# Optimization experiments

Hardware: AMD Instinct MI355X
Metric: run time of the kernel (lower is better)

## Reference

```python
import jax, jax.numpy as jnp
import numpy as np

HID = 512
NB = 20
N = 65536
EPS = 1e-5


def layer_norm(x, g, b):
    m = jnp.mean(x, axis=-1, keepdims=True)
    v = jnp.mean(jnp.square(x - m), axis=-1, keepdims=True)
    return (x - m) * jax.lax.rsqrt(v + EPS) * g + b


def setup_inputs() -> dict:
    key = jax.random.key(0)
    ks = jax.random.split(key, 8)
    s = 0.02
    return {
        "x": jax.random.normal(ks[0], (N, 2), dtype=jnp.float32),
        "in_w": jax.random.normal(ks[1], (2, HID), dtype=jnp.float32) * s,
        "in_b": jnp.zeros((HID,), jnp.float32),
        "ln1_g": jnp.ones((NB, HID), jnp.float32),
        "ln1_b": jnp.zeros((NB, HID), jnp.float32),
        "fc1_w": jax.random.normal(ks[2], (NB, HID, HID), dtype=jnp.float32) * s,
        "fc1_b": jnp.zeros((NB, HID), jnp.float32),
        "ln2_g": jnp.ones((NB, HID), jnp.float32),
        "ln2_b": jnp.zeros((NB, HID), jnp.float32),
        "fc2_w": jax.random.normal(ks[3], (NB, HID, HID), dtype=jnp.float32) * s,
        "fc2_b": jnp.zeros((NB, HID), jnp.float32),
        "out_ln_g": jnp.ones((HID,), jnp.float32),
        "out_ln_b": jnp.zeros((HID,), jnp.float32),
        "out_w": jax.random.normal(ks[4], (HID, 1), dtype=jnp.float32) * s,
        "out_b": jnp.zeros((1,), jnp.float32),
    }


def reference(x, in_w, in_b, ln1_g, ln1_b, fc1_w, fc1_b, ln2_g, ln2_b,
              fc2_w, fc2_b, out_ln_g, out_ln_b, out_w, out_b):
    # in_proj + SiLU: [N,2] @ [2,HID]
    h = jax.nn.silu(x @ in_w + in_b)

    def block(h, p):
        g1, b1, w1, c1, g2, b2, w2, c2 = p
        t = jax.nn.silu(layer_norm(h, g1, b1) @ w1 + c1)
        t = layer_norm(t, g2, b2) @ w2 + c2
        return h + t, None

    h, _ = jax.lax.scan(block, h, (ln1_g, ln1_b, fc1_w, fc1_b,
                                   ln2_g, ln2_b, fc2_w, fc2_b))
    h = jax.nn.silu(layer_norm(h, out_ln_g, out_ln_b))
    return h @ out_w + out_b  # [N, 1]
```

## Files before the change

### kernel.cpp

```cpp
#include <hip/hip_runtime.h>
#include <hip/hip_bf16.h>


typedef float  fvec4 __attribute__((ext_vector_type(4)));
typedef __bf16 bvec8 __attribute__((ext_vector_type(8)));

#define HN_STRIDE 520
#define WCHUNK    16384
#define SMEM_BYTES (64*HN_STRIDE*2 + 64*8)
#define WPK_USHORTS ((size_t)20*2*16*WCHUNK)

__device__ __forceinline__ unsigned int f2bf(float v) {
    unsigned int u = __float_as_uint(v);
    return (u + 0x7fffu + ((u >> 16) & 1u)) >> 16;
}
__device__ __forceinline__ unsigned int pkbf(float a, float b) {
    __hip_bfloat162 t = __float22bfloat162_rn(make_float2(a, b));
    unsigned int r;
    __builtin_memcpy(&r, &t, 4);
    return r;
}
__device__ __forceinline__ float silu_f(float v) {
    return v * (1.0f / (1.0f + __expf(-v)));
}

__global__ __launch_bounds__(256) void pack_weights(
        const float* __restrict__ w1, const float* __restrict__ w2,
        const float* __restrict__ g1, const float* __restrict__ g2,
        unsigned short* __restrict__ pk) {
    int tid = blockIdx.x * 256 + threadIdx.x;
    int l  = tid & 63;
    int f  = tid >> 6;
    int t  = f & 1;
    int kc = (f >> 1) & 15;
    int w  = (f >> 5) & 15;
    int g  = (f >> 9) & 1;
    int b  = f >> 10;
    const float* src = g ? w2 : w1;
    const float* gs  = (g ? g2 : g1) + b * 512;
    int k0 = kc * 32 + (l >> 4) * 8;
    int n  = w * 32 + (l & 15) * 2 + t;
    const float* s = src + ((size_t)b * 512 + k0) * 512 + n;
    unsigned int r[4];
#pragma unroll
    for (int j = 0; j < 4; ++j) {
        float ga = gs[k0 + 2 * j];
        float gb = gs[k0 + 2 * j + 1];
        unsigned int lo = f2bf(ga * s[(size_t)(2*j) * 512]);
        unsigned int hi = f2bf(gb * s[(size_t)(2*j + 1) * 512]);
        r[j] = lo | (hi << 16);
    }
    *(uint4*)(pk + (size_t)tid * 8) = make_uint4(r[0], r[1], r[2], r[3]);
}

__global__ __launch_bounds__(512) void make_uv(
        const float* __restrict__ w1, const float* __restrict__ w2,
        const float* __restrict__ g1, const float* __restrict__ bl1,
        const float* __restrict__ cb1,
        const float* __restrict__ g2, const float* __restrict__ bl2,
        const float* __restrict__ cb2,
        float* __restrict__ uv) {
    int b = blockIdx.x >> 1, slot = blockIdx.x & 1, n = threadIdx.x;
    const float* W  = (slot ? w2 : w1) + (size_t)b * 512 * 512;
    const float* g  = (slot ? g2 : g1) + b * 512;
    const float* bl = (slot ? bl2 : bl1) + b * 512;
    const float* cb = (slot ? cb2 : cb1) + b * 512;
    float u = 0.f, v = 0.f;
    for (int j = 0; j < 512; ++j) {
        float wv = W[(size_t)j * 512 + n];
        u = fmaf(g[j], wv, u);
        v = fmaf(bl[j], wv, v);
    }
    uv[((b * 2 + slot) * 2 + 0) * 512 + n] = u;
    uv[((b * 2 + slot) * 2 + 1) * 512 + n] = v + cb[n];
}

__device__ __forceinline__ void acc_u32(unsigned int u, float& s, float& ss) {
    float lo = __uint_as_float(u << 16);
    float hi = __uint_as_float(u & 0xFFFF0000u);
    s += lo + hi;
    ss = __builtin_fmaf(lo, lo, ss);
    ss = __builtin_fmaf(hi, hi, ss);
}

__device__ __forceinline__ void gemm_red(
        fvec4 acc[4][2], const unsigned short* hn,
        const unsigned short* __restrict__ wp, uint4 pre0, uint4 pre1,
        float2* mv, int l, int c, int q, int tid) {
    const uint4* wp4 = (const uint4*)wp;
    const int r = tid >> 4, j = tid & 15;
    float s = 0.f, ss = 0.f;
#pragma unroll
    for (int kc = 0; kc < 16; ++kc) {
        bvec8 a[4], b0, b1;
#pragma unroll
        for (int rb = 0; rb < 4; ++rb)
            a[rb] = *(const bvec8*)(hn + (rb * 16 + c) * HN_STRIDE + kc * 32 + q * 8);
        if (kc == 0) {
            __builtin_memcpy(&b0, &pre0, 16);
            __builtin_memcpy(&b1, &pre1, 16);
        } else {
            uint4 r0 = wp4[(kc * 2 + 0) * 64 + l];
            uint4 r1 = wp4[(kc * 2 + 1) * 64 + l];
            __builtin_memcpy(&b0, &r0, 16);
            __builtin_memcpy(&b1, &r1, 16);
        }
        if (kc >= 4 && kc < 8) {
            uint4 pv = *(const uint4*)(hn + r * HN_STRIDE + (j + 16 * (kc - 4)) * 8);
            acc_u32(pv.x, s, ss); acc_u32(pv.y, s, ss);
            acc_u32(pv.z, s, ss); acc_u32(pv.w, s, ss);
        }
#pragma unroll
        for (int rb = 0; rb < 4; ++rb) {
            acc[rb][0] = __builtin_amdgcn_mfma_f32_16x16x32_bf16(a[rb], b0, acc[rb][0], 0, 0, 0);
            acc[rb][1] = __builtin_amdgcn_mfma_f32_16x16x32_bf16(a[rb], b1, acc[rb][1], 0, 0, 0);
        }
    }
    s += __shfl_xor(s, 1); ss += __shfl_xor(ss, 1);
    s += __shfl_xor(s, 2); ss += __shfl_xor(ss, 2);
    s += __shfl_xor(s, 4); ss += __shfl_xor(ss, 4);
    s += __shfl_xor(s, 8); ss += __shfl_xor(ss, 8);
    if (j == 0) {
        float mean = s * (1.f / 512.f);
        float var  = ss * (1.f / 512.f) - mean * mean;
        mv[r] = make_float2(mean, rsqrtf(var + 1e-5f));
    }
}

__device__ __forceinline__ void reduce_mv_hn(const unsigned short* hn,
                                             float2* mv, int tid) {
    int r = tid >> 4, j = tid & 15;
    float s = 0.f, ss = 0.f;
#pragma unroll
    for (int u = 0; u < 4; ++u) {
        uint4 pv = *(const uint4*)(hn + r * HN_STRIDE + (j + 16 * u) * 8);
        acc_u32(pv.x, s, ss); acc_u32(pv.y, s, ss);
        acc_u32(pv.z, s, ss); acc_u32(pv.w, s, ss);
    }
    s += __shfl_xor(s, 1); ss += __shfl_xor(ss, 1);
    s += __shfl_xor(s, 2); ss += __shfl_xor(ss, 2);
    s += __shfl_xor(s, 4); ss += __shfl_xor(ss, 4);
    s += __shfl_xor(s, 8); ss += __shfl_xor(ss, 8);
    if (j == 0) {
        float mean = s * (1.f / 512.f);
        float var  = ss * (1.f / 512.f) - mean * mean;
        mv[r] = make_float2(mean, rsqrtf(var + 1e-5f));
    }
}

__global__ __launch_bounds__(1024, 4) void mlp_fused(
        const float* __restrict__ x,
        const float* __restrict__ in_w,  const float* __restrict__ in_b,
        const float* __restrict__ out_ln_g, const float* __restrict__ out_ln_b,
        const float* __restrict__ out_w, const float* __restrict__ out_b,
        const unsigned short* __restrict__ wpk,
        const float* __restrict__ uv,
        float* __restrict__ out) {
    extern __shared__ char smem[];
    unsigned short* hn = (unsigned short*)smem;
    float* hnf = (float*)smem;
    float2* mv = (float2*)(smem + 64 * HN_STRIDE * 2);

    const int tid = threadIdx.x;
    const int w = tid >> 6;
    const int l = tid & 63, c = l & 15, q = l >> 4;
    const int colbase = w * 32 + c * 2;
    const int row0 = blockIdx.x * 64;

    float h[4][4][2];

    {
        float2 iw0 = *(const float2*)(in_w + colbase);
        float2 iw1 = *(const float2*)(in_w + 512 + colbase);
        float2 ib  = *(const float2*)(in_b + colbase);
#pragma unroll
        for (int rb = 0; rb < 4; ++rb)
#pragma unroll
            for (int i = 0; i < 4; ++i) {
                int row = rb * 16 + q * 4 + i;
                float2 xv = *(const float2*)(x + (size_t)(row0 + row) * 2);
                h[rb][i][0] = silu_f(xv.x * iw0.x + xv.y * iw1.x + ib.x);
                h[rb][i][1] = silu_f(xv.x * iw0.y + xv.y * iw1.y + ib.y);
            }
    }

    for (int b = 0; b < 20; ++b) {
        const unsigned short* wp1 = wpk + ((size_t)(b * 2 + 0) * 16 + w) * WCHUNK;
        const unsigned short* wp2 = wpk + ((size_t)(b * 2 + 1) * 16 + w) * WCHUNK;
        float2 u1  = *(const float2*)(uv + ((b * 2 + 0) * 2 + 0) * 512 + colbase);
        float2 vc1 = *(const float2*)(uv + ((b * 2 + 0) * 2 + 1) * 512 + colbase);
        float2 u2  = *(const float2*)(uv + ((b * 2 + 1) * 2 + 0) * 512 + colbase);
        float2 vc2 = *(const float2*)(uv + ((b * 2 + 1) * 2 + 1) * 512 + colbase);

        uint4 pre0 = ((const uint4*)wp1)[l];
        uint4 pre1 = ((const uint4*)wp1)[64 + l];
#pragma unroll
        for (int rb = 0; rb < 4; ++rb)
#pragma unroll
            for (int i = 0; i < 4; ++i) {
                int row = rb * 16 + q * 4 + i;
                *(unsigned int*)(hn + row * HN_STRIDE + colbase) =
                    pkbf(h[rb][i][0], h[rb][i][1]);
            }
        __syncthreads();

        fvec4 acc[4][2];
#pragma unroll
        for (int rb = 0; rb < 4; ++rb)
#pragma unroll
            for (int t = 0; t < 2; ++t) acc[rb][t] = (fvec4){0.f, 0.f, 0.f, 0.f};
        gemm_red(acc, hn, wp1, pre0, pre1, mv, l, c, q, tid);
        __syncthreads();

        pre0 = ((const uint4*)wp2)[l];
        pre1 = ((const uint4*)wp2)[64 + l];
#pragma unroll
        for (int rb = 0; rb < 4; ++rb)
#pragma unroll
            for (int i = 0; i < 4; ++i) {
                int row = rb * 16 + q * 4 + i;
                float2 m = mv[row];
                float minv = -m.x * m.y;
                float t0 = silu_f(__builtin_fmaf(acc[rb][0][i], m.y,
                                  __builtin_fmaf(minv, u1.x, vc1.x)));
                float t1 = silu_f(__builtin_fmaf(acc[rb][1][i], m.y,
                                  __builtin_fmaf(minv, u1.y, vc1.y)));
                *(unsigned int*)(hn + row * HN_STRIDE + colbase) = pkbf(t0, t1);
            }
        __syncthreads();

#pragma unroll
        for (int rb = 0; rb < 4; ++rb)
#pragma unroll
            for (int t = 0; t < 2; ++t) acc[rb][t] = (fvec4){0.f, 0.f, 0.f, 0.f};
        gemm_red(acc, hn, wp2, pre0, pre1, mv, l, c, q, tid);
        __syncthreads();

#pragma unroll
        for (int rb = 0; rb < 4; ++rb)
#pragma unroll
            for (int i = 0; i < 4; ++i) {
                int row = rb * 16 + q * 4 + i;
                float2 m = mv[row];
                float minv = -m.x * m.y;
                h[rb][i][0] = __builtin_fmaf(acc[rb][0][i], m.y,
                    h[rb][i][0] + __builtin_fmaf(minv, u2.x, vc2.x));
                h[rb][i][1] = __builtin_fmaf(acc[rb][1][i], m.y,
                    h[rb][i][1] + __builtin_fmaf(minv, u2.y, vc2.y));
            }
    }

#pragma unroll
    for (int rb = 0; rb < 4; ++rb)
#pragma unroll
        for (int i = 0; i < 4; ++i) {
            int row = rb * 16 + q * 4 + i;
            *(unsigned int*)(hn + row * HN_STRIDE + colbase) =
                pkbf(h[rb][i][0], h[rb][i][1]);
        }
    __syncthreads();
    reduce_mv_hn(hn, mv, tid);
    __syncthreads();
    {
        float2 og = *(const float2*)(out_ln_g + colbase);
        float2 ob = *(const float2*)(out_ln_b + colbase);
        float2 ow = *(const float2*)(out_w + colbase);
        const int pcol = w * 16 + c;
#pragma unroll
    for (int rb = 0; rb < 4; ++rb)
#pragma unroll
            for (int i = 0; i < 4; ++i) {
                int row = rb * 16 + q * 4 + i;
                float2 m = mv[row];
                float v0 = (h[rb][i][0] - m.x) * m.y * og.x + ob.x;
                float v1 = (h[rb][i][1] - m.x) * m.y * og.y + ob.y;
                hnf[pcol * 65 + row] = silu_f(v0) * ow.x + silu_f(v1) * ow.y;
            }
    }
    __syncthreads();
    {
        int r = tid >> 4, j = tid & 15;
        float s = 0.f;
#pragma unroll
        for (int u = 0; u < 16; ++u)
            s += hnf[(j + 16 * u) * 65 + r];
        s += __shfl_xor(s, 1);
        s += __shfl_xor(s, 2);
        s += __shfl_xor(s, 4);
        s += __shfl_xor(s, 8);
        if (j == 0) out[row0 + r] = s + out_b[0];
    }
}

extern "C" void kernel_launch(void* const* d_in, const int* in_sizes, int n_in,
                              void* d_out, int out_size, void* d_ws, size_t ws_size,
                              hipStream_t stream) {
    const float* x        = (const float*)d_in[0];
    const float* in_w     = (const float*)d_in[1];
    const float* in_b     = (const float*)d_in[2];
    const float* ln1_g    = (const float*)d_in[3];
    const float* ln1_b    = (const float*)d_in[4];
    const float* fc1_w    = (const float*)d_in[5];
    const float* fc1_b    = (const float*)d_in[6];
    const float* ln2_g    = (const float*)d_in[7];
    const float* ln2_b    = (const float*)d_in[8];
    const float* fc2_w    = (const float*)d_in[9];
    const float* fc2_b    = (const float*)d_in[10];
    const float* out_ln_g = (const float*)d_in[11];
    const float* out_ln_b = (const float*)d_in[12];
    const float* out_w    = (const float*)d_in[13];
    const float* out_b    = (const float*)d_in[14];
    float* out = (float*)d_out;
    unsigned short* wpk = (unsigned short*)d_ws;
    float* uv = (float*)((char*)d_ws + WPK_USHORTS * 2);

    (void)hipFuncSetAttribute((const void*)mlp_fused,
                              hipFuncAttributeMaxDynamicSharedMemorySize, SMEM_BYTES);

    pack_weights<<<5120, 256, 0, stream>>>(fc1_w, fc2_w, ln1_g, ln2_g, wpk);
    make_uv<<<40, 512, 0, stream>>>(fc1_w, fc2_w, ln1_g, ln1_b, fc1_b,
                                    ln2_g, ln2_b, fc2_b, uv);
    mlp_fused<<<1024, 1024, SMEM_BYTES, stream>>>(
        x, in_w, in_b, out_ln_g, out_ln_b, out_w, out_b, wpk, uv, out);
}
```

Before: 1.776 ms.

## Compute LayerNorm partial sums at emit time and prefetch next block weights

Each thread now computes partial sum and sum-of-squares for its two output values when writing activations, reduces them over 4 lanes with shuffles, and stores them to a new shared-memory plane. The GEMM and final reduction then read 64 partials per row instead of re-reading and unpacking the whole bf16 row. Statistics now come from fp32 values rather than bf16-rounded ones. The first weight chunk of the next block is also prefetched before the residual update. This trades extra shuffles and shared-memory footprint (which may affect occupancy) for fewer LDS reads and less ALU work in the GEMM loop.

Measured after the change: 2.754 ms. 55.0% more time.

```diff
diff --git a/kernel.cpp b/kernel.cpp
--- a/kernel.cpp
+++ b/kernel.cpp
@@ -6,8 +6,9 @@
 typedef __bf16 bvec8 __attribute__((ext_vector_type(8)));
 
 #define HN_STRIDE 520
+#define PL_STRIDE 66
 #define WCHUNK    16384
-#define SMEM_BYTES (64*HN_STRIDE*2 + 64*8)
+#define SMEM_BYTES (64*HN_STRIDE*2 + 64*PL_STRIDE*8 + 64*8)
 #define WPK_USHORTS ((size_t)20*2*16*WCHUNK)
 
 __device__ __forceinline__ unsigned int f2bf(float v) {
@@ -75,18 +76,10 @@
     uv[((b * 2 + slot) * 2 + 1) * 512 + n] = v + cb[n];
 }
 
-__device__ __forceinline__ void acc_u32(unsigned int u, float& s, float& ss) {
-    float lo = __uint_as_float(u << 16);
-    float hi = __uint_as_float(u & 0xFFFF0000u);
-    s += lo + hi;
-    ss = __builtin_fmaf(lo, lo, ss);
-    ss = __builtin_fmaf(hi, hi, ss);
-}
-
 __device__ __forceinline__ void gemm_red(
         fvec4 acc[4][2], const unsigned short* hn,
         const unsigned short* __restrict__ wp, uint4 pre0, uint4 pre1,
-        float2* mv, int l, int c, int q, int tid) {
+        const float2* plane2, float2* mv, int l, int c, int q, int tid) {
     const uint4* wp4 = (const uint4*)wp;
     const int r = tid >> 4, j = tid & 15;
     float s = 0.f, ss = 0.f;
@@ -105,10 +98,15 @@
             __builtin_memcpy(&b0, &r0, 16);
             __builtin_memcpy(&b1, &r1, 16);
         }
-        if (kc >= 4 && kc < 8) {
-            uint4 pv = *(const uint4*)(hn + r * HN_STRIDE + (j + 16 * (kc - 4)) * 8);
-            acc_u32(pv.x, s, ss); acc_u32(pv.y, s, ss);
-            acc_u32(pv.z, s, ss); acc_u32(pv.w, s, ss);
+        if (kc == 4) {
+            float2 p0 = plane2[r * PL_STRIDE + j * 4 + 0];
+            float2 p1 = plane2[r * PL_STRIDE + j * 4 + 1];
+            s += p0.x + p1.x; ss += p0.y + p1.y;
+        }
+        if (kc == 5) {
+            float2 p0 = plane2[r * PL_STRIDE + j * 4 + 2];
+            float2 p1 = plane2[r * PL_STRIDE + j * 4 + 3];
+            s += p0.x + p1.x; ss += p0.y + p1.y;
         }
 #pragma unroll
         for (int rb = 0; rb < 4; ++rb) {
@@ -127,15 +125,14 @@
     }
 }
 
-__device__ __forceinline__ void reduce_mv_hn(const unsigned short* hn,
-                                             float2* mv, int tid) {
+__device__ __forceinline__ void reduce_mv_plane(const float2* plane2,
+                                                float2* mv, int tid) {
     int r = tid >> 4, j = tid & 15;
     float s = 0.f, ss = 0.f;
 #pragma unroll
-    for (int u = 0; u < 4; ++u) {
-        uint4 pv = *(const uint4*)(hn + r * HN_STRIDE + (j + 16 * u) * 8);
-        acc_u32(pv.x, s, ss); acc_u32(pv.y, s, ss);
-        acc_u32(pv.z, s, ss); acc_u32(pv.w, s, ss);
+    for (int k = 0; k < 4; ++k) {
+        float2 p = plane2[r * PL_STRIDE + j * 4 + k];
+        s += p.x; ss += p.y;
     }
     s += __shfl_xor(s, 1); ss += __shfl_xor(ss, 1);
     s += __shfl_xor(s, 2); ss += __shfl_xor(ss, 2);
@@ -159,15 +156,27 @@
     extern __shared__ char smem[];
     unsigned short* hn = (unsigned short*)smem;
     float* hnf = (float*)smem;
-    float2* mv = (float2*)(smem + 64 * HN_STRIDE * 2);
+    float2* plane2 = (float2*)(smem + 64 * HN_STRIDE * 2);
+    float2* mv = (float2*)(smem + 64 * HN_STRIDE * 2 + 64 * PL_STRIDE * 8);
 
     const int tid = threadIdx.x;
     const int w = tid >> 6;
     const int l = tid & 63, c = l & 15, q = l >> 4;
     const int colbase = w * 32 + c * 2;
     const int row0 = blockIdx.x * 64;
+    const int grp = w * 4 + (c >> 2);
+    const bool gw = (c & 3) == 0;
 
     float h[4][4][2];
+
+    auto emit = [&](int row, float v0, float v1) {
+        *(unsigned int*)(hn + row * HN_STRIDE + colbase) = pkbf(v0, v1);
+        float s  = v0 + v1;
+        float ss = __builtin_fmaf(v0, v0, v1 * v1);
+        s += __shfl_xor(s, 1); ss += __shfl_xor(ss, 1);
+        s += __shfl_xor(s, 2); ss += __shfl_xor(ss, 2);
+        if (gw) plane2[row * PL_STRIDE + grp] = make_float2(s, ss);
+    };
 
     {
         float2 iw0 = *(const float2*)(in_w + colbase);
@@ -181,27 +190,22 @@
                 float2 xv = *(const float2*)(x + (size_t)(row0 + row) * 2);
                 h[rb][i][0] = silu_f(xv.x * iw0.x + xv.y * iw1.x + ib.x);
                 h[rb][i][1] = silu_f(xv.x * iw0.y + xv.y * iw1.y + ib.y);
+                emit(row, h[rb][i][0], h[rb][i][1]);
             }
     }
+    uint4 pre0 = ((const uint4*)(wpk + ((size_t)0 * 16 + w) * WCHUNK))[l];
+    uint4 pre1 = ((const uint4*)(wpk + ((size_t)0 * 16 + w) * WCHUNK))[64 + l];
 
     for (int b = 0; b < 20; ++b) {
         const unsigned short* wp1 = wpk + ((size_t)(b * 2 + 0) * 16 + w) * WCHUNK;
         const unsigned short* wp2 = wpk + ((size_t)(b * 2 + 1) * 16 + w) * WCHUNK;
+        int bn = (b < 19) ? (b + 1) * 2 : 38;
+        const unsigned short* wpn = wpk + ((size_t)bn * 16 + w) * WCHUNK;
         float2 u1  = *(const float2*)(uv + ((b * 2 + 0) * 2 + 0) * 512 + colbase);
         float2 vc1 = *(const float2*)(uv + ((b * 2 + 0) * 2 + 1) * 512 + colbase);
         float2 u2  = *(const float2*)(uv + ((b * 2 + 1) * 2 + 0) * 512 + colbase);
         float2 vc2 = *(const float2*)(uv + ((b * 2 + 1) * 2 + 1) * 512 + colbase);
 
-        uint4 pre0 = ((const uint4*)wp1)[l];
-        uint4 pre1 = ((const uint4*)wp1)[64 + l];
-#pragma unroll
-        for (int rb = 0; rb < 4; ++rb)
-#pragma unroll
-            for (int i = 0; i < 4; ++i) {
-                int row = rb * 16 + q * 4 + i;
-                *(unsigned int*)(hn + row * HN_STRIDE + colbase) =
-                    pkbf(h[rb][i][0], h[rb][i][1]);
-            }
         __syncthreads();
 
         fvec4 acc[4][2];
@@ -209,7 +213,7 @@
         for (int rb = 0; rb < 4; ++rb)
 #pragma unroll
             for (int t = 0; t < 2; ++t) acc[rb][t] = (fvec4){0.f, 0.f, 0.f, 0.f};
-        gemm_red(acc, hn, wp1, pre0, pre1, mv, l, c, q, tid);
+        gemm_red(acc, hn, wp1, pre0, pre1, plane2, mv, l, c, q, tid);
         __syncthreads();
 
         pre0 = ((const uint4*)wp2)[l];
@@ -225,7 +229,7 @@
                                   __builtin_fmaf(minv, u1.x, vc1.x)));
                 float t1 = silu_f(__builtin_fmaf(acc[rb][1][i], m.y,
                                   __builtin_fmaf(minv, u1.y, vc1.y)));
-                *(unsigned int*)(hn + row * HN_STRIDE + colbase) = pkbf(t0, t1);
+                emit(row, t0, t1);
             }
         __syncthreads();
 
@@ -233,9 +237,11 @@
         for (int rb = 0; rb < 4; ++rb)
 #pragma unroll
             for (int t = 0; t < 2; ++t) acc[rb][t] = (fvec4){0.f, 0.f, 0.f, 0.f};
-        gemm_red(acc, hn, wp2, pre0, pre1, mv, l, c, q, tid);
+        gemm_red(acc, hn, wp2, pre0, pre1, plane2, mv, l, c, q, tid);
         __syncthreads();
 
+        pre0 = ((const uint4*)wpn)[l];
+        pre1 = ((const uint4*)wpn)[64 + l];
 #pragma unroll
         for (int rb = 0; rb < 4; ++rb)
 #pragma unroll
@@ -247,19 +253,12 @@
                     h[rb][i][0] + __builtin_fmaf(minv, u2.x, vc2.x));
                 h[rb][i][1] = __builtin_fmaf(acc[rb][1][i], m.y,
                     h[rb][i][1] + __builtin_fmaf(minv, u2.y, vc2.y));
+                emit(row, h[rb][i][0], h[rb][i][1]);
             }
     }
 
-#pragma unroll
-    for (int rb = 0; rb < 4; ++rb)
-#pragma unroll
-        for (int i = 0; i < 4; ++i) {
-            int row = rb * 16 + q * 4 + i;
-            *(unsigned int*)(hn + row * HN_STRIDE + colbase) =
-                pkbf(h[rb][i][0], h[rb][i][1]);
-        }
     __syncthreads();
-    reduce_mv_hn(hn, mv, tid);
+    reduce_mv_plane(plane2, mv, tid);
     __syncthreads();
     {
         float2 og = *(const float2*)(out_ln_g + colbase);
@@ -267,7 +266,7 @@
         float2 ow = *(const float2*)(out_w + colbase);
         const int pcol = w * 16 + c;
 #pragma unroll
-    for (int rb = 0; rb < 4; ++rb)
+        for (int rb = 0; rb < 4; ++rb)
 #pragma unroll
             for (int i = 0; i < 4; ++i) {
                 int row = rb * 16 + q * 4 + i;
```
